# Kernel tuning notes

Hardware: AMD Instinct MI355X
Metric: run time of the kernel (lower is better)

## Reference

```python
import jax, jax.numpy as jnp
import numpy as np

N = 30000   # num_nodes
E = 480000  # num_edges (avg degree 16)
R = 8       # num_relations
B = 4       # num_bases
H = 128     # h_dim
OUT = 128   # out_dim


def setup_inputs() -> dict:
    key = jax.random.key(0)
    ks = jax.random.split(key, 16)
    s = 0.05
    return {
        "x": jnp.arange(N, dtype=jnp.int32),
        "src": jax.random.randint(ks[0], (E,), 0, N, dtype=jnp.int32),
        "dst": jax.random.randint(ks[1], (E,), 0, N, dtype=jnp.int32),
        "rel": jax.random.randint(ks[2], (E,), 0, R, dtype=jnp.int32),
        "norm": jax.random.uniform(ks[3], (E,), dtype=jnp.float32),
        # input layer (featureless: in_feat == num_nodes, basis decomposition)
        "V_in": jax.random.normal(ks[4], (B, N, H), dtype=jnp.float32) * s,
        "comp_in": jax.random.normal(ks[5], (R, B), dtype=jnp.float32) * 0.5,
        "bias_in": jnp.zeros((H,), dtype=jnp.float32),
        # hidden layer
        "V_h": jax.random.normal(ks[6], (B, H, H), dtype=jnp.float32) * s,
        "comp_h": jax.random.normal(ks[7], (R, B), dtype=jnp.float32) * 0.5,
        "bias_h": jnp.zeros((H,), dtype=jnp.float32),
        # output layer
        "V_out": jax.random.normal(ks[8], (B, H, OUT), dtype=jnp.float32) * s,
        "comp_out": jax.random.normal(ks[9], (R, B), dtype=jnp.float32) * 0.5,
        "bias_out": jnp.zeros((OUT,), dtype=jnp.float32),
        # GlobalAttentionPooling gate_nn: Linear(out_dim, 1)
        "gate_W": jax.random.normal(ks[10], (OUT, 1), dtype=jnp.float32) * s,
        "gate_b": jnp.zeros((1,), dtype=jnp.float32),
    }


def _rgc_dense(h, src, dst, rel, norm, V, comp, bias):
    """RelGraphConv (basis) for dense node features h: [N, in]."""
    c = comp[rel]          # [E, B] per-edge basis coefficients
    hs = h[src]            # [E, in] gather source features
    m = jnp.zeros((hs.shape[0], V.shape[-1]), dtype=h.dtype)
    for b in range(V.shape[0]):  # small fixed loop over bases
        m = m + c[:, b:b + 1] * (hs @ V[b])
    m = m * norm[:, None]
    return jax.ops.segment_sum(m, dst, num_segments=N) + bias


def _rgc_idfeat(x, src, dst, rel, norm, V, comp, bias):
    """Input RelGraphConv with node-ID features (one-hot == row gather)."""
    Wfull = jnp.einsum('rb,bno->rno', comp, V)    # [R, N, H]
    m = Wfull[rel, x[src]] * norm[:, None]        # [E, H]
    return jax.ops.segment_sum(m, dst, num_segments=N) + bias


def reference(x, src, dst, rel, norm,
              V_in, comp_in, bias_in,
              V_h, comp_h, bias_h,
              V_out, comp_out, bias_out,
              gate_W, gate_b):
    h = _rgc_idfeat(x, src, dst, rel, norm, V_in, comp_in, bias_in)
    h = jax.nn.relu(h)  # dropout p=0.0 -> identity
    h = _rgc_dense(h, src, dst, rel, norm, V_h, comp_h, bias_h)
    h = jax.nn.relu(h)
    h = _rgc_dense(h, src, dst, rel, norm, V_out, comp_out, bias_out)
    # GlobalAttentionPooling (single graph): softmax over nodes
    gate = jax.nn.softmax(h @ gate_W + gate_b, axis=0)  # [N, 1]
    return jnp.sum(gate * h, axis=0)  # [OUT]
```

## Files before the change

### kernel.cpp

```cpp
#include <hip/hip_runtime.h>
#include <hip/hip_bf16.h>

#define NN 30000
#define EE 480000
#define RR 8
#define BB 4
#define HH 128
#define NH (NN * HH)
#define NCAP 30016
#define CH 8
#define CSLOT 16
#define NN64 (NN * 64)

typedef __attribute__((ext_vector_type(8))) short short8;
typedef __attribute__((ext_vector_type(4))) float float4v;

__device__ __forceinline__ unsigned short f2bf(float f) {
    union { float f; unsigned int i; } c; c.f = f;
    unsigned int r = c.i + 0x7fffu + ((c.i >> 16) & 1u);
    return (unsigned short)(r >> 16);
}
__device__ __forceinline__ float bflo(unsigned int v) {
    union { unsigned int i; float f; } c; c.i = v << 16; return c.f;
}
__device__ __forceinline__ float bfhi(unsigned int v) {
    union { unsigned int i; float f; } c; c.i = v & 0xFFFF0000u; return c.f;
}
__device__ __forceinline__ unsigned int packbf(float a, float b) {
    return (unsigned int)f2bf(a) | ((unsigned int)f2bf(b) << 16);
}

#define SCAT_BLOCKS 469
#define TBL_BLOCKS 1875
#define BTF_BLOCKS 512
__global__ __launch_bounds__(256)
void k_mix(const int* __restrict__ dst, const int* __restrict__ src,
           const int* __restrict__ rel, const float* __restrict__ norm,
           int* __restrict__ cnt, unsigned int* __restrict__ meta,
           const float* __restrict__ V_in, const float* __restrict__ comp_in,
           unsigned int* __restrict__ table_u,
           const float* __restrict__ V_h, const float* __restrict__ V_o,
           unsigned short* __restrict__ Btf_h, unsigned short* __restrict__ Btf_o,
           float* __restrict__ scal, float* __restrict__ out) {
    int bid = blockIdx.x;
    if (bid < SCAT_BLOCKS) {
        int c = bid & 7;
        int base = bid * 1024 + threadIdx.x;
        int d[4]; unsigned int u[4]; bool ok[4];
#pragma unroll
        for (int e = 0; e < 4; ++e) {
            int i = base + e * 256;
            ok[e] = i < EE;
            d[e] = ok[e] ? dst[i] : 0;
            int sv = ok[e] ? src[i] : 0;
            int rv = ok[e] ? rel[i] : 0;
            float nv = ok[e] ? norm[i] : 0.f;
            unsigned int nq = (unsigned int)(nv * 16383.f + 0.5f);
            u[e] = (nq << 18) | ((unsigned int)rv << 15) | (unsigned int)sv;
        }
        int p[4];
#pragma unroll
        for (int e = 0; e < 4; ++e)
            if (ok[e]) p[e] = atomicAdd(&cnt[c * NCAP + d[e]], 1);
#pragma unroll
        for (int e = 0; e < 4; ++e)
            if (ok[e] && p[e] < CSLOT)
                meta[(c * NCAP + d[e]) * CSLOT + p[e]] = u[e];
    } else if (bid < SCAT_BLOCKS + TBL_BLOCKS) {
        int idx = ((bid - SCAT_BLOCKS) * 256 + threadIdx.x) * 8;
        float4v va[4], vb[4];
#pragma unroll
        for (int b = 0; b < 4; ++b) {
            va[b] = *(const float4v*)(V_in + b * NH + idx);
            vb[b] = *(const float4v*)(V_in + b * NH + idx + 4);
        }
#pragma unroll
        for (int r = 0; r < RR; ++r) {
            float c0 = comp_in[r * 4 + 0], c1 = comp_in[r * 4 + 1];
            float c2 = comp_in[r * 4 + 2], c3 = comp_in[r * 4 + 3];
            float4v oa = c0 * va[0] + c1 * va[1] + c2 * va[2] + c3 * va[3];
            float4v ob = c0 * vb[0] + c1 * vb[1] + c2 * vb[2] + c3 * vb[3];
            uint4 sv;
            sv.x = packbf(oa[0], oa[1]); sv.y = packbf(oa[2], oa[3]);
            sv.z = packbf(ob[0], ob[1]); sv.w = packbf(ob[2], ob[3]);
            *(uint4*)(table_u + (r * NH + idx) / 2) = sv;
        }
    } else {
        if (bid == SCAT_BLOCKS + TBL_BLOCKS) {
            if (threadIdx.x == 0) scal[0] = 0.f;
            if (threadIdx.x >= 128) out[threadIdx.x - 128] = 0.f;
        }
        int idx = (bid - SCAT_BLOCKS - TBL_BLOCKS) * 256 + threadIdx.x;
        int which = idx >> 16;
        int local = idx & 0xFFFF;
        int j = local >> 9;
        int k = local & 511;
        const float* V = which ? V_o : V_h;
        unsigned short* W = which ? Btf_o : Btf_h;
        int half = k >> 8, kk = (k >> 5) & 7, kq = (k >> 3) & 3, e = k & 7;
        int c = j >> 4, mr = j & 15;
        int fi = half * 32768 + ((((kk * 4 + kq) * 8 + c) * 16 + mr) * 8 + e);
        W[fi] = f2bf(V[k * 128 + j]);
    }
}

__global__ __launch_bounds__(256)
void k_agg1(const unsigned int* __restrict__ table_u, const int* __restrict__ cnt,
            const unsigned int* __restrict__ meta, const float* __restrict__ bias,
            unsigned int* __restrict__ h1u) {
    __shared__ int s_row[4][128];
    __shared__ float s_wt[4][128];
    int tid = threadIdx.x;
    int w = tid >> 6, lane = tid & 63;
    int d = blockIdx.x * 4 + w;
    int s = lane & 15, cg = lane >> 4;
    int cn0 = cnt[cg * NCAP + d]; if (cn0 > CSLOT) cn0 = CSLOT;
    int cn1 = cnt[(cg + 4) * NCAP + d]; if (cn1 > CSLOT) cn1 = CSLOT;
    bool v0 = s < cn0, v1 = s < cn1;
    unsigned int m0 = v0 ? meta[(cg * NCAP + d) * CSLOT + s] : 0u;
    unsigned int m1 = v1 ? meta[((cg + 4) * NCAP + d) * CSLOT + s] : 0u;
    unsigned long long bal0 = __ballot(v0);
    unsigned long long bal1 = __ballot(v1);
    unsigned long long below = (1ULL << lane) - 1ULL;
    int tot0 = __popcll(bal0);
    if (v0) {
        int idx = __popcll(bal0 & below);
        s_row[w][idx] = (int)(((m0 >> 15) & 7u) * (unsigned int)NN64 + (m0 & 0x7FFFu) * 64u);
        s_wt[w][idx] = (float)(m0 >> 18) * (1.f / 16383.f);
    }
    if (v1) {
        int idx = tot0 + __popcll(bal1 & below);
        s_row[w][idx] = (int)(((m1 >> 15) & 7u) * (unsigned int)NN64 + (m1 & 0x7FFFu) * 64u);
        s_wt[w][idx] = (float)(m1 >> 18) * (1.f / 16383.f);
    }
    int cn = tot0 + __popcll(bal1);
    __syncthreads();
    float a0 = 0.f, a1 = 0.f, b0 = 0.f, b1 = 0.f;
    int j = 0;
    for (; j + 8 <= cn; j += 8) {
        int r[8]; float wt[8]; unsigned int v[8];
#pragma unroll
        for (int e = 0; e < 8; ++e) { r[e] = s_row[w][j + e]; wt[e] = s_wt[w][j + e]; }
#pragma unroll
        for (int e = 0; e < 8; ++e) v[e] = table_u[r[e] + lane];
#pragma unroll
        for (int e = 0; e < 8; ++e) {
            if (e & 1) { b0 += wt[e] * bflo(v[e]); b1 += wt[e] * bfhi(v[e]); }
            else       { a0 += wt[e] * bflo(v[e]); a1 += wt[e] * bfhi(v[e]); }
        }
    }
    for (; j + 4 <= cn; j += 4) {
        int r[4]; float wt[4]; unsigned int v[4];
#pragma unroll
        for (int e = 0; e < 4; ++e) { r[e] = s_row[w][j + e]; wt[e] = s_wt[w][j + e]; }
#pragma unroll
        for (int e = 0; e < 4; ++e) v[e] = table_u[r[e] + lane];
#pragma unroll
        for (int e = 0; e < 4; ++e) {
            if (e & 1) { b0 += wt[e] * bflo(v[e]); b1 += wt[e] * bfhi(v[e]); }
            else       { a0 += wt[e] * bflo(v[e]); a1 += wt[e] * bfhi(v[e]); }
        }
    }
    for (; j < cn; ++j) {
        int r0 = s_row[w][j];
        float w0 = s_wt[w][j];
        unsigned int v0 = table_u[r0 + lane];
        a0 += w0 * bflo(v0); a1 += w0 * bfhi(v0);
    }
    a0 += b0 + bias[2 * lane];
    a1 += b1 + bias[2 * lane + 1];
    a0 = fmaxf(a0, 0.f); a1 = fmaxf(a1, 0.f);
    h1u[d * 64 + lane] = packbf(a0, a1);
}

__global__ __launch_bounds__(256)
void k_aggb(const unsigned int* __restrict__ hu, const int* __restrict__ cnt,
            const unsigned int* __restrict__ meta, const float* __restrict__ comp,
            unsigned int* __restrict__ gu) {
    __shared__ int s_off[4][128];
    __shared__ float s_w0[4][128], s_w1[4][128], s_w2[4][128], s_w3[4][128];
    int tid = threadIdx.x;
    int w = tid >> 6, lane = tid & 63;
    int d = blockIdx.x * 4 + w;
    int s = lane & 15, cg = lane >> 4;
    int cn0 = cnt[cg * NCAP + d]; if (cn0 > CSLOT) cn0 = CSLOT;
    int cn1 = cnt[(cg + 4) * NCAP + d]; if (cn1 > CSLOT) cn1 = CSLOT;
    bool v0 = s < cn0, v1 = s < cn1;
    unsigned int m0 = v0 ? meta[(cg * NCAP + d) * CSLOT + s] : 0u;
    unsigned int m1 = v1 ? meta[((cg + 4) * NCAP + d) * CSLOT + s] : 0u;
    unsigned long long bal0 = __ballot(v0);
    unsigned long long bal1 = __ballot(v1);
    unsigned long long below = (1ULL << lane) - 1ULL;
    int tot0 = __popcll(bal0);
    if (v0) {
        int idx = __popcll(bal0 & below);
        int r4 = (int)((m0 >> 15) & 7u) * 4;
        float nm = (float)(m0 >> 18) * (1.f / 16383.f);
        s_off[w][idx] = (int)((m0 & 0x7FFFu) << 6);
        s_w0[w][idx] = comp[r4 + 0] * nm; s_w1[w][idx] = comp[r4 + 1] * nm;
        s_w2[w][idx] = comp[r4 + 2] * nm; s_w3[w][idx] = comp[r4 + 3] * nm;
    }
    if (v1) {
        int idx = tot0 + __popcll(bal1 & below);
        int r4 = (int)((m1 >> 15) & 7u) * 4;
        float nm = (float)(m1 >> 18) * (1.f / 16383.f);
        s_off[w][idx] = (int)((m1 & 0x7FFFu) << 6);
        s_w0[w][idx] = comp[r4 + 0] * nm; s_w1[w][idx] = comp[r4 + 1] * nm;
        s_w2[w][idx] = comp[r4 + 2] * nm; s_w3[w][idx] = comp[r4 + 3] * nm;
    }
    int cn = tot0 + __popcll(bal1);
    __syncthreads();
    float a00 = 0, a01 = 0, a10 = 0, a11 = 0, a20 = 0, a21 = 0, a30 = 0, a31 = 0;
    int j = 0;
    for (; j + 8 <= cn; j += 8) {
        int o[8]; unsigned int v[8];
#pragma unroll
        for (int e = 0; e < 8; ++e) o[e] = s_off[w][j + e];
#pragma unroll
        for (int e = 0; e < 8; ++e) v[e] = hu[o[e] + lane];
#pragma unroll
        for (int e = 0; e < 8; ++e) {
            float w0 = s_w0[w][j + e], w1 = s_w1[w][j + e];
            float w2 = s_w2[w][j + e], w3 = s_w3[w][j + e];
            float f0 = bflo(v[e]), f1 = bfhi(v[e]);
            a00 += w0 * f0; a01 += w0 * f1;
            a10 += w1 * f0; a11 += w1 * f1;
            a20 += w2 * f0; a21 += w2 * f1;
            a30 += w3 * f0; a31 += w3 * f1;
        }
    }
    for (; j < cn; ++j) {
        int off = s_off[w][j];
        float w0 = s_w0[w][j], w1 = s_w1[w][j];
        float w2 = s_w2[w][j], w3 = s_w3[w][j];
        unsigned int v = hu[off + lane];
        float f0 = bflo(v), f1 = bfhi(v);
        a00 += w0 * f0; a01 += w0 * f1;
        a10 += w1 * f0; a11 += w1 * f1;
        a20 += w2 * f0; a21 += w2 * f1;
        a30 += w3 * f0; a31 += w3 * f1;
    }
    gu[d * 256 +       lane] = packbf(a00, a01);
    gu[d * 256 +  64 + lane] = packbf(a10, a11);
    gu[d * 256 + 128 + lane] = packbf(a20, a21);
    gu[d * 256 + 192 + lane] = packbf(a30, a31);
}

__global__ __launch_bounds__(256)
void k_gemm2(const unsigned short* __restrict__ A, const unsigned short* __restrict__ Btf,
             const float* __restrict__ bias, unsigned int* __restrict__ outu, int relu,
             const float* __restrict__ gW, const float* __restrict__ gb,
             float* __restrict__ wexp, float* __restrict__ scal) {
    __shared__ unsigned short bsm[32768];
    int tid = threadIdx.x;
    int w = tid >> 6, lane = tid & 63;
    int mr = lane & 15, kq = lane >> 4;
    int m0 = (blockIdx.x * 4 + w) * 16;
    float4v z = {0.f, 0.f, 0.f, 0.f};
    float4v acc[8];
#pragma unroll
    for (int c = 0; c < 8; ++c) acc[c] = z;
    const unsigned short* arow = A + (m0 + mr) * 512 + kq * 8;
#pragma unroll
    for (int half = 0; half < 2; ++half) {
        {
            const uint4* sb = (const uint4*)(Btf + half * 32768);
            uint4* db = (uint4*)bsm;
#pragma unroll
            for (int i = 0; i < 16; ++i) db[tid + i * 256] = sb[tid + i * 256];
        }
        __syncthreads();
#pragma unroll
        for (int kk = 0; kk < 8; ++kk) {
            short8 a = *(const short8*)(arow + half * 256 + kk * 32);
#pragma unroll
            for (int c = 0; c < 8; ++c) {
                short8 b = *(const short8*)(bsm + ((((kk * 4 + kq) * 8 + c) * 16 + mr) << 3));
                acc[c] = __builtin_amdgcn_mfma_f32_16x16x32_bf16(a, b, acc[c], 0, 0, 0);
            }
        }
        __syncthreads();
    }
    float* lds = (float*)bsm;
#pragma unroll
    for (int c = 0; c < 8; ++c)
#pragma unroll
        for (int i = 0; i < 4; ++i)
            lds[(w * 16 + kq * 4 + i) * 132 + c * 16 + mr] = acc[c][i];
    __syncthreads();
    float b0 = bias[2 * lane], b1 = bias[2 * lane + 1];
    float gw0 = 0.f, gw1 = 0.f, gb0 = 0.f, lsum = 0.f;
    if (wexp) { gw0 = gW[2 * lane]; gw1 = gW[2 * lane + 1]; gb0 = gb[0]; }
    for (int it = 0; it < 16; ++it) {
        int node = m0 + it;
        if (node < NN) {
            float f0 = lds[(w * 16 + it) * 132 + 2 * lane] + b0;
            float f1 = lds[(w * 16 + it) * 132 + 2 * lane + 1] + b1;
            if (relu) { f0 = fmaxf(f0, 0.f); f1 = fmaxf(f1, 0.f); }
            if (wexp) {
                float p = f0 * gw0 + f1 * gw1;
#pragma unroll
                for (int off = 32; off; off >>= 1) p += __shfl_down(p, off);
                if (lane == 0) {
                    float we = __expf(p + gb0);
                    wexp[node] = we;
                    lsum += we;
                }
            }
            outu[node * 64 + lane] = packbf(f0, f1);
        }
    }
    if (wexp && lane == 0) atomicAdd(&scal[0], lsum);
}

__global__ __launch_bounds__(256)
void k_out(const unsigned int* __restrict__ h3u, const float* __restrict__ wexp,
           const float* __restrict__ scal, float* __restrict__ out) {
    __shared__ float s_acc[4][128];
    int tid = threadIdx.x;
    int w = tid >> 6, h = tid & 63;
    int n0 = blockIdx.x * 256 + w * 64;
    int n1 = n0 + 64; if (n1 > NN) n1 = NN;
    float inv = 1.f / scal[0];
    float a0 = 0.f, a1 = 0.f, b0 = 0.f, b1 = 0.f;
    int n = n0;
    for (; n + 2 <= n1; n += 2) {
        float wa = wexp[n] * inv;
        float wb = wexp[n + 1] * inv;
        unsigned int va = h3u[n * 64 + h];
        unsigned int vb = h3u[(n + 1) * 64 + h];
        a0 += wa * bflo(va); a1 += wa * bfhi(va);
        b0 += wb * bflo(vb); b1 += wb * bfhi(vb);
    }
    for (; n < n1; ++n) {
        float wa = wexp[n] * inv;
        unsigned int va = h3u[n * 64 + h];
        a0 += wa * bflo(va); a1 += wa * bfhi(va);
    }
    s_acc[w][2 * h] = a0 + b0;
    s_acc[w][2 * h + 1] = a1 + b1;
    __syncthreads();
    if (tid < 128) {
        float t = s_acc[0][tid] + s_acc[1][tid] + s_acc[2][tid] + s_acc[3][tid];
        atomicAdd(&out[tid], t);
    }
}

extern "C" void kernel_launch(void* const* d_in, const int* in_sizes, int n_in,
                              void* d_out, int out_size, void* d_ws, size_t ws_size,
                              hipStream_t stream) {
    const int* src = (const int*)d_in[1];
    const int* dst = (const int*)d_in[2];
    const int* rel = (const int*)d_in[3];
    const float* norm = (const float*)d_in[4];
    const float* V_in = (const float*)d_in[5];
    const float* comp_in = (const float*)d_in[6];
    const float* bias_in = (const float*)d_in[7];
    const float* V_h = (const float*)d_in[8];
    const float* comp_h = (const float*)d_in[9];
    const float* bias_h = (const float*)d_in[10];
    const float* V_out = (const float*)d_in[11];
    const float* comp_out = (const float*)d_in[12];
    const float* bias_out = (const float*)d_in[13];
    const float* gate_W = (const float*)d_in[14];
    const float* gate_b = (const float*)d_in[15];
    float* out = (float*)d_out;

    char* ws = (char*)d_ws;
    unsigned short* table = (unsigned short*)ws;
    unsigned short* g = (unsigned short*)ws;
    unsigned int* h1u = (unsigned int*)(ws + 61440000);
    unsigned int* h2u = (unsigned int*)(ws + 69120000);
    unsigned int* h3u = (unsigned int*)(ws + 76800000);
    unsigned short* Btf_h = (unsigned short*)(ws + 84480000);
    unsigned short* Btf_o = (unsigned short*)(ws + 84611072);
    int* cnt = (int*)(ws + 84742144);
    unsigned int* meta = (unsigned int*)(ws + 85702656);
    float* wexp = (float*)(ws + 101070848);
    float* scal = (float*)(ws + 101190848);

    hipMemsetAsync(cnt, 0, CH * NCAP * sizeof(int), stream);
    k_mix<<<SCAT_BLOCKS + TBL_BLOCKS + BTF_BLOCKS, 256, 0, stream>>>(
        dst, src, rel, norm, cnt, meta, V_in, comp_in, (unsigned int*)table,
        V_h, V_out, Btf_h, Btf_o, scal, out);

    k_agg1<<<NN / 4, 256, 0, stream>>>((const unsigned int*)table, cnt, meta, bias_in, h1u);

    k_aggb<<<NN / 4, 256, 0, stream>>>(h1u, cnt, meta, comp_h, (unsigned int*)g);
    k_gemm2<<<469, 256, 0, stream>>>(g, Btf_h, bias_h, h2u, 1,
                                     (const float*)nullptr, (const float*)nullptr,
                                     (float*)nullptr, (float*)nullptr);

    k_aggb<<<NN / 4, 256, 0, stream>>>(h2u, cnt, meta, comp_out, (unsigned int*)g);
    k_gemm2<<<469, 256, 0, stream>>>(g, Btf_o, bias_out, h3u, 0, gate_W, gate_b,
                                     wexp, scal);

    k_out<<<(NN + 255) / 256, 256, 0, stream>>>(h3u, wexp, scal, out);
}
```

Baseline: 290.6 us.

## Fuse basis aggregation and GEMM into one kernel per hidden layer

Merges the per-node basis aggregation and the following bf16 MFMA GEMM into one kernel that builds a 32-row aggregated tile in swizzled LDS and multiplies it straight away. This removes the global write and re-read of the intermediate [N,512] bf16 buffer and one launch per layer. Weights are now read from global memory per wave instead of being staged in LDS, and the per-edge coefficients are recomputed from packed metadata and an LDS copy of comp. Each 512-thread block handles only 32 rows, so the GEMM has little reuse of the B matrix.

```diff
diff --git a/kernel.cpp b/kernel.cpp
--- a/kernel.cpp
+++ b/kernel.cpp
@@ -173,129 +173,120 @@
     h1u[d * 64 + lane] = packbf(a0, a1);
 }
 
-__global__ __launch_bounds__(256)
-void k_aggb(const unsigned int* __restrict__ hu, const int* __restrict__ cnt,
-            const unsigned int* __restrict__ meta, const float* __restrict__ comp,
-            unsigned int* __restrict__ gu) {
-    __shared__ int s_off[4][128];
-    __shared__ float s_w0[4][128], s_w1[4][128], s_w2[4][128], s_w3[4][128];
+#define FT_ROWS 32
+#define FT_BLOCKS (NCAP / FT_ROWS)
+__global__ __launch_bounds__(512)
+void k_fused(const unsigned int* __restrict__ hu, const int* __restrict__ cnt,
+             const unsigned int* __restrict__ meta, const float* __restrict__ comp,
+             const unsigned short* __restrict__ Btf, const float* __restrict__ bias,
+             unsigned int* __restrict__ outu, int relu,
+             const float* __restrict__ gW, const float* __restrict__ gb,
+             float* __restrict__ wexp, float* __restrict__ scal) {
+    __shared__ __align__(16) unsigned short Asm[FT_ROWS * 512];
+    __shared__ unsigned int s_meta[8][128];
+    __shared__ float4v s_comp4[8];
+    __shared__ float s_ls[8];
     int tid = threadIdx.x;
     int w = tid >> 6, lane = tid & 63;
-    int d = blockIdx.x * 4 + w;
+    if (tid < 32) ((float*)s_comp4)[tid] = comp[tid];
+    __syncthreads();
+    int m0 = blockIdx.x * FT_ROWS;
     int s = lane & 15, cg = lane >> 4;
-    int cn0 = cnt[cg * NCAP + d]; if (cn0 > CSLOT) cn0 = CSLOT;
-    int cn1 = cnt[(cg + 4) * NCAP + d]; if (cn1 > CSLOT) cn1 = CSLOT;
-    bool v0 = s < cn0, v1 = s < cn1;
-    unsigned int m0 = v0 ? meta[(cg * NCAP + d) * CSLOT + s] : 0u;
-    unsigned int m1 = v1 ? meta[((cg + 4) * NCAP + d) * CSLOT + s] : 0u;
-    unsigned long long bal0 = __ballot(v0);
-    unsigned long long bal1 = __ballot(v1);
     unsigned long long below = (1ULL << lane) - 1ULL;
-    int tot0 = __popcll(bal0);
-    if (v0) {
-        int idx = __popcll(bal0 & below);
-        int r4 = (int)((m0 >> 15) & 7u) * 4;
-        float nm = (float)(m0 >> 18) * (1.f / 16383.f);
-        s_off[w][idx] = (int)((m0 & 0x7FFFu) << 6);
-        s_w0[w][idx] = comp[r4 + 0] * nm; s_w1[w][idx] = comp[r4 + 1] * nm;
-        s_w2[w][idx] = comp[r4 + 2] * nm; s_w3[w][idx] = comp[r4 + 3] * nm;
-    }
-    if (v1) {
-        int idx = tot0 + __popcll(bal1 & below);
-        int r4 = (int)((m1 >> 15) & 7u) * 4;
-        float nm = (float)(m1 >> 18) * (1.f / 16383.f);
-        s_off[w][idx] = (int)((m1 & 0x7FFFu) << 6);
-        s_w0[w][idx] = comp[r4 + 0] * nm; s_w1[w][idx] = comp[r4 + 1] * nm;
-        s_w2[w][idx] = comp[r4 + 2] * nm; s_w3[w][idx] = comp[r4 + 3] * nm;
-    }
-    int cn = tot0 + __popcll(bal1);
-    __syncthreads();
-    float a00 = 0, a01 = 0, a10 = 0, a11 = 0, a20 = 0, a21 = 0, a30 = 0, a31 = 0;
-    int j = 0;
-    for (; j + 8 <= cn; j += 8) {
-        int o[8]; unsigned int v[8];
-#pragma unroll
-        for (int e = 0; e < 8; ++e) o[e] = s_off[w][j + e];
-#pragma unroll
-        for (int e = 0; e < 8; ++e) v[e] = hu[o[e] + lane];
-#pragma unroll
-        for (int e = 0; e < 8; ++e) {
-            float w0 = s_w0[w][j + e], w1 = s_w1[w][j + e];
-            float w2 = s_w2[w][j + e], w3 = s_w3[w][j + e];
-            float f0 = bflo(v[e]), f1 = bfhi(v[e]);
+    for (int t = 0; t < 4; ++t) {
+        int d = m0 + w * 4 + t;
+        int cn0 = cnt[cg * NCAP + d]; if (cn0 > CSLOT) cn0 = CSLOT;
+        int cn1 = cnt[(cg + 4) * NCAP + d]; if (cn1 > CSLOT) cn1 = CSLOT;
+        bool v0 = s < cn0, v1 = s < cn1;
+        unsigned int mm0 = v0 ? meta[(cg * NCAP + d) * CSLOT + s] : 0u;
+        unsigned int mm1 = v1 ? meta[((cg + 4) * NCAP + d) * CSLOT + s] : 0u;
+        unsigned long long bal0 = __ballot(v0);
+        unsigned long long bal1 = __ballot(v1);
+        int tot0 = __popcll(bal0);
+        if (v0) s_meta[w][__popcll(bal0 & below)] = mm0;
+        if (v1) s_meta[w][tot0 + __popcll(bal1 & below)] = mm1;
+        int cn = tot0 + __popcll(bal1);
+        float a00 = 0, a01 = 0, a10 = 0, a11 = 0, a20 = 0, a21 = 0, a30 = 0, a31 = 0;
+        int j = 0;
+        for (; j + 8 <= cn; j += 8) {
+            unsigned int mm[8]; unsigned int v[8];
+#pragma unroll
+            for (int e = 0; e < 8; ++e) mm[e] = s_meta[w][j + e];
+#pragma unroll
+            for (int e = 0; e < 8; ++e) v[e] = hu[((mm[e] & 0x7FFFu) << 6) + lane];
+#pragma unroll
+            for (int e = 0; e < 8; ++e) {
+                float4v wv = s_comp4[(mm[e] >> 15) & 7u];
+                float nm = (float)(mm[e] >> 18) * (1.f / 16383.f);
+                float w0 = wv[0] * nm, w1 = wv[1] * nm;
+                float w2 = wv[2] * nm, w3 = wv[3] * nm;
+                float f0 = bflo(v[e]), f1 = bfhi(v[e]);
+                a00 += w0 * f0; a01 += w0 * f1;
+                a10 += w1 * f0; a11 += w1 * f1;
+                a20 += w2 * f0; a21 += w2 * f1;
+                a30 += w3 * f0; a31 += w3 * f1;
+            }
+        }
+        for (; j < cn; ++j) {
+            unsigned int mm = s_meta[w][j];
+            unsigned int v = hu[((mm & 0x7FFFu) << 6) + lane];
+            float4v wv = s_comp4[(mm >> 15) & 7u];
+            float nm = (float)(mm >> 18) * (1.f / 16383.f);
+            float w0 = wv[0] * nm, w1 = wv[1] * nm;
+            float w2 = wv[2] * nm, w3 = wv[3] * nm;
+            float f0 = bflo(v), f1 = bfhi(v);
             a00 += w0 * f0; a01 += w0 * f1;
             a10 += w1 * f0; a11 += w1 * f1;
             a20 += w2 * f0; a21 += w2 * f1;
             a30 += w3 * f0; a31 += w3 * f1;
         }
-    }
-    for (; j < cn; ++j) {
-        int off = s_off[w][j];
-        float w0 = s_w0[w][j], w1 = s_w1[w][j];
-        float w2 = s_w2[w][j], w3 = s_w3[w][j];
-        unsigned int v = hu[off + lane];
-        float f0 = bflo(v), f1 = bfhi(v);
-        a00 += w0 * f0; a01 += w0 * f1;
-        a10 += w1 * f0; a11 += w1 * f1;
-        a20 += w2 * f0; a21 += w2 * f1;
-        a30 += w3 * f0; a31 += w3 * f1;
-    }
-    gu[d * 256 +       lane] = packbf(a00, a01);
-    gu[d * 256 +  64 + lane] = packbf(a10, a11);
-    gu[d * 256 + 128 + lane] = packbf(a20, a21);
-    gu[d * 256 + 192 + lane] = packbf(a30, a31);
-}
-
-__global__ __launch_bounds__(256)
-void k_gemm2(const unsigned short* __restrict__ A, const unsigned short* __restrict__ Btf,
-             const float* __restrict__ bias, unsigned int* __restrict__ outu, int relu,
-             const float* __restrict__ gW, const float* __restrict__ gb,
-             float* __restrict__ wexp, float* __restrict__ scal) {
-    __shared__ unsigned short bsm[32768];
-    int tid = threadIdx.x;
-    int w = tid >> 6, lane = tid & 63;
+        int row = w * 4 + t;
+        char* base = (char*)Asm + row * 1024;
+        unsigned int sw = (unsigned int)((row & 7) << 4);
+        *(unsigned int*)(base + ((0u * 256u + lane * 4u) ^ sw)) = packbf(a00, a01);
+        *(unsigned int*)(base + ((1u * 256u + lane * 4u) ^ sw)) = packbf(a10, a11);
+        *(unsigned int*)(base + ((2u * 256u + lane * 4u) ^ sw)) = packbf(a20, a21);
+        *(unsigned int*)(base + ((3u * 256u + lane * 4u) ^ sw)) = packbf(a30, a31);
+    }
+    __syncthreads();
     int mr = lane & 15, kq = lane >> 4;
-    int m0 = (blockIdx.x * 4 + w) * 16;
+    int rw = w & 1, cb = w >> 1;
+    int arow = rw * 16 + mr;
+    const char* abase = (const char*)Asm + arow * 1024;
+    unsigned int swr = (unsigned int)((arow & 7) << 4);
     float4v z = {0.f, 0.f, 0.f, 0.f};
-    float4v acc[8];
-#pragma unroll
-    for (int c = 0; c < 8; ++c) acc[c] = z;
-    const unsigned short* arow = A + (m0 + mr) * 512 + kq * 8;
+    float4v acc0 = z, acc1 = z;
 #pragma unroll
     for (int half = 0; half < 2; ++half) {
-        {
-            const uint4* sb = (const uint4*)(Btf + half * 32768);
-            uint4* db = (uint4*)bsm;
-#pragma unroll
-            for (int i = 0; i < 16; ++i) db[tid + i * 256] = sb[tid + i * 256];
-        }
-        __syncthreads();
 #pragma unroll
         for (int kk = 0; kk < 8; ++kk) {
-            short8 a = *(const short8*)(arow + half * 256 + kk * 32);
-#pragma unroll
-            for (int c = 0; c < 8; ++c) {
-                short8 b = *(const short8*)(bsm + ((((kk * 4 + kq) * 8 + c) * 16 + mr) << 3));
-                acc[c] = __builtin_amdgcn_mfma_f32_16x16x32_bf16(a, b, acc[c], 0, 0, 0);
-            }
-        }
-        __syncthreads();
-    }
-    float* lds = (float*)bsm;
-#pragma unroll
-    for (int c = 0; c < 8; ++c)
-#pragma unroll
-        for (int i = 0; i < 4; ++i)
-            lds[(w * 16 + kq * 4 + i) * 132 + c * 16 + mr] = acc[c][i];
+            short8 a = *(const short8*)(abase +
+                        ((unsigned int)(half * 512 + kk * 64 + kq * 16) ^ swr));
+            int c0 = cb * 2;
+            short8 bv0 = *(const short8*)(Btf + half * 32768 +
+                          ((((kk * 4 + kq) * 8 + c0) * 16 + mr) << 3));
+            short8 bv1 = *(const short8*)(Btf + half * 32768 +
+                          ((((kk * 4 + kq) * 8 + c0 + 1) * 16 + mr) << 3));
+            acc0 = __builtin_amdgcn_mfma_f32_16x16x32_bf16(a, bv0, acc0, 0, 0, 0);
+            acc1 = __builtin_amdgcn_mfma_f32_16x16x32_bf16(a, bv1, acc1, 0, 0, 0);
+        }
+    }
+    __syncthreads();
+    float* lds = (float*)Asm;
+#pragma unroll
+    for (int i = 0; i < 4; ++i) {
+        lds[(rw * 16 + kq * 4 + i) * 132 + (cb * 2) * 16 + mr] = acc0[i];
+        lds[(rw * 16 + kq * 4 + i) * 132 + (cb * 2 + 1) * 16 + mr] = acc1[i];
+    }
     __syncthreads();
     float b0 = bias[2 * lane], b1 = bias[2 * lane + 1];
     float gw0 = 0.f, gw1 = 0.f, gb0 = 0.f, lsum = 0.f;
     if (wexp) { gw0 = gW[2 * lane]; gw1 = gW[2 * lane + 1]; gb0 = gb[0]; }
-    for (int it = 0; it < 16; ++it) {
-        int node = m0 + it;
+    for (int it = 0; it < 4; ++it) {
+        int node = m0 + w * 4 + it;
         if (node < NN) {
-            float f0 = lds[(w * 16 + it) * 132 + 2 * lane] + b0;
-            float f1 = lds[(w * 16 + it) * 132 + 2 * lane + 1] + b1;
+            float f0 = lds[(w * 4 + it) * 132 + 2 * lane] + b0;
+            float f1 = lds[(w * 4 + it) * 132 + 2 * lane + 1] + b1;
             if (relu) { f0 = fmaxf(f0, 0.f); f1 = fmaxf(f1, 0.f); }
             if (wexp) {
                 float p = f0 * gw0 + f1 * gw1;
@@ -310,7 +301,15 @@
             outu[node * 64 + lane] = packbf(f0, f1);
         }
     }
-    if (wexp && lane == 0) atomicAdd(&scal[0], lsum);
+    if (wexp) {
+        if (lane == 0) s_ls[w] = lsum;
+        __syncthreads();
+        if (tid == 0) {
+            float t = s_ls[0] + s_ls[1] + s_ls[2] + s_ls[3]
+                    + s_ls[4] + s_ls[5] + s_ls[6] + s_ls[7];
+            atomicAdd(&scal[0], t);
+        }
+    }
 }
 
 __global__ __launch_bounds__(256)
@@ -368,7 +367,6 @@
 
     char* ws = (char*)d_ws;
     unsigned short* table = (unsigned short*)ws;
-    unsigned short* g = (unsigned short*)ws;
     unsigned int* h1u = (unsigned int*)(ws + 61440000);
     unsigned int* h2u = (unsigned int*)(ws + 69120000);
     unsigned int* h3u = (unsigned int*)(ws + 76800000);
@@ -386,14 +384,12 @@
 
     k_agg1<<<NN / 4, 256, 0, stream>>>((const unsigned int*)table, cnt, meta, bias_in, h1u);
 
-    k_aggb<<<NN / 4, 256, 0, stream>>>(h1u, cnt, meta, comp_h, (unsigned int*)g);
-    k_gemm2<<<469, 256, 0, stream>>>(g, Btf_h, bias_h, h2u, 1,
-                                     (const float*)nullptr, (const float*)nullptr,
-                                     (float*)nullptr, (float*)nullptr);
-
-    k_aggb<<<NN / 4, 256, 0, stream>>>(h2u, cnt, meta, comp_out, (unsigned int*)g);
-    k_gemm2<<<469, 256, 0, stream>>>(g, Btf_o, bias_out, h3u, 0, gate_W, gate_b,
-                                     wexp, scal);
+    k_fused<<<FT_BLOCKS, 512, 0, stream>>>(h1u, cnt, meta, comp_h, Btf_h, bias_h, h2u, 1,
+                                           (const float*)nullptr, (const float*)nullptr,
+                                           (float*)nullptr, (float*)nullptr);
+
+    k_fused<<<FT_BLOCKS, 512, 0, stream>>>(h2u, cnt, meta, comp_out, Btf_o, bias_out, h3u, 0,
+                                           gate_W, gate_b, wexp, scal);
 
     k_out<<<(NN + 255) / 256, 256, 0, stream>>>(h3u, wexp, scal, out);
 }
```

Result: faster. 283.7 us (-2.4%).
